# Kernel tuning notes

Measured on AMD Instinct MI355X. Metric: run time of the kernel, lower is better.

Reference implementation:

```python
import jax, jax.numpy as jnp
import numpy as np

EPS = 1e-5

def setup_inputs() -> dict:
    key = jax.random.key(0)
    ks = jax.random.split(key, 5)
    B, C_clip, Hc, Wc = 8, 768, 24, 24
    C_rs, Hr, Wr = 256, 64, 64
    clip_feat = jax.random.normal(ks[0], (B, C_clip, Hc, Wc), dtype=jnp.float32)
    rs_feat = jax.random.normal(ks[1], (B, C_rs, Hr, Wr), dtype=jnp.float32)
    ln_gamma = jnp.ones((C_clip,), dtype=jnp.float32)
    ln_beta = jnp.zeros((C_clip,), dtype=jnp.float32)
    W = jax.random.normal(ks[2], (C_rs, C_clip), dtype=jnp.float32) * (1.0 / np.sqrt(C_clip))
    b = jax.random.normal(ks[3], (C_rs,), dtype=jnp.float32) * 0.01
    alpha = jnp.array([0.5], dtype=jnp.float32)
    return {"clip_feat": clip_feat, "rs_feat": rs_feat, "ln_gamma": ln_gamma,
            "ln_beta": ln_beta, "W": W, "b": b, "alpha": alpha}

def reference(clip_feat, rs_feat, ln_gamma, ln_beta, W, b, alpha):
    B, C_clip, Hc, Wc = clip_feat.shape
    _, C_rs, Hr, Wr = rs_feat.shape
    # tokens: [B, N_clip, C_clip]
    clip_flat = clip_feat.reshape(B, C_clip, Hc * Wc).transpose(0, 2, 1)
    mu = jnp.mean(clip_flat, axis=-1, keepdims=True)
    var = jnp.var(clip_flat, axis=-1, keepdims=True)
    clip_norm = (clip_flat - mu) * jax.lax.rsqrt(var + EPS) * ln_gamma + ln_beta
    # projection to rs_dim: [B, N_clip, C_rs]
    clip_proj = jnp.einsum('bnc,dc->bnd', clip_norm, W) + b
    # rs tokens: [B, N_rs, C_rs]
    rs_flat = rs_feat.reshape(B, C_rs, Hr * Wr).transpose(0, 2, 1)
    # attn_map: [B, N_clip, N_rs], softmax over N_clip (axis=1)
    attn = jnp.einsum('bnd,bmd->bnm', clip_proj, rs_flat)
    attn = jax.nn.softmax(attn, axis=1)
    # attended: [B, N_rs, C_rs]
    attended = jnp.einsum('bnm,bnd->bmd', attn, clip_proj)
    attended = attended.transpose(0, 2, 1).reshape(B, C_rs, Hr, Wr)
    return rs_feat + alpha * attended
```

## Files before the change

### kernel.cpp

```cpp
#include <hip/hip_runtime.h>
#include <hip/hip_bf16.h>

#define EPSF 1e-5f
#define SM_OFF 60.0f

typedef short short8 __attribute__((ext_vector_type(8)));
typedef float f32x4 __attribute__((ext_vector_type(4)));

__device__ __forceinline__ short f2bf(float x) {
    __hip_bfloat16 h = __float2bfloat16(x);
    return reinterpret_cast<short&>(h);
}
__device__ __forceinline__ float bf2f(short s) {
    __hip_bfloat16 h = reinterpret_cast<__hip_bfloat16&>(s);
    return __bfloat162float(h);
}
__device__ __forceinline__ unsigned int pk2(float lo, float hi) {
    return (unsigned int)(unsigned short)f2bf(lo)
         | ((unsigned int)(unsigned short)f2bf(hi) << 16);
}
__device__ __forceinline__ void gload_lds16(const short* g, short* lds) {
    __builtin_amdgcn_global_load_lds(
        (const __attribute__((address_space(1))) unsigned int*)g,
        (__attribute__((address_space(3))) unsigned int*)lds,
        16, 0, 0);
}

__global__ __launch_bounds__(256) void w_pack_kernel(
    const float* __restrict__ W,
    short* __restrict__ Wp_hi,
    short* __restrict__ Wp_lo)
{
    int t = blockIdx.x * 256 + threadIdx.x;
    int l15 = t & 15;
    int g   = (t >> 4) & 3;
    int kt  = (t >> 6) % 24;
    int nt  = t / 1536;
    const float* src = W + (size_t)(16 * nt + l15) * 768 + 32 * kt + 8 * g;
    short8 h8, l8;
    #pragma unroll
    for (int j = 0; j < 8; ++j) {
        float w = src[j];
        short h = f2bf(w);
        h8[j] = h;
        l8[j] = f2bf(w - bf2f(h));
    }
    *reinterpret_cast<short8*>(Wp_hi + (size_t)t * 8) = h8;
    *reinterpret_cast<short8*>(Wp_lo + (size_t)t * 8) = l8;
}

__global__ __launch_bounds__(512) void ln_proj_kernel(
    const float* __restrict__ clip,
    const float* __restrict__ gamma,
    const float* __restrict__ beta,
    const short* __restrict__ Wp_hi,
    const short* __restrict__ Wp_lo,
    const float* __restrict__ bias,
    short* __restrict__ proj,
    short* __restrict__ projT)
{
    __shared__ short xh[16][776];
    __shared__ short xl[16][776];
    __shared__ float redA[8][16];
    __shared__ float redB[8][16];
    __shared__ float muS[16], rsS[16];

    const int tid = threadIdx.x;
    const int bb = blockIdx.x >> 1;
    const int dh = blockIdx.x & 1;
    const int b  = bb / 36;
    const int n0 = (bb % 36) * 16;
    const int nl = tid & 15;
    const int cg = tid >> 4;
    const int w  = tid >> 6;
    const int l  = tid & 63;
    const int l15 = l & 15;
    const int g  = l >> 4;

    const float* base = clip + (size_t)b * 768 * 576 + n0 + nl;

    float x[24];
    float s1 = 0.f, s2 = 0.f;
    #pragma unroll
    for (int i = 0; i < 24; ++i) {
        x[i] = base[(size_t)(cg + 32 * i) * 576];
        s1 += x[i]; s2 += x[i] * x[i];
    }
    s1 += __shfl_xor(s1, 16); s2 += __shfl_xor(s2, 16);
    s1 += __shfl_xor(s1, 32); s2 += __shfl_xor(s2, 32);
    if (g == 0) { redA[w][l15] = s1; redB[w][l15] = s2; }
    __syncthreads();
    if (tid < 16) {
        float a = 0.f, q = 0.f;
        #pragma unroll
        for (int k = 0; k < 8; ++k) { a += redA[k][tid]; q += redB[k][tid]; }
        float mu = a * (1.f / 768.f);
        float var = q * (1.f / 768.f) - mu * mu;
        muS[tid] = mu; rsS[tid] = rsqrtf(var + EPSF);
    }
    __syncthreads();
    {
        float mu = muS[nl], rsg = rsS[nl];
        #pragma unroll
        for (int i = 0; i < 24; ++i) {
            int c = cg + 32 * i;
            float y = (x[i] - mu) * rsg * gamma[c] + beta[c];
            short hh = f2bf(y);
            xh[nl][c] = hh;
            xl[nl][c] = f2bf(y - bf2f(hh));
        }
    }
    __syncthreads();

    const int nt = 8 * dh + w;
    f32x4 acc = f32x4{0.f, 0.f, 0.f, 0.f};
    for (int kt = 0; kt < 24; ++kt) {
        short8 ah = *reinterpret_cast<const short8*>(&xh[l15][32 * kt + 8 * g]);
        short8 al = *reinterpret_cast<const short8*>(&xl[l15][32 * kt + 8 * g]);
        size_t off = ((size_t)((nt * 24 + kt) * 64 + l)) * 8;
        short8 bh = *reinterpret_cast<const short8*>(Wp_hi + off);
        short8 bl = *reinterpret_cast<const short8*>(Wp_lo + off);
        acc = __builtin_amdgcn_mfma_f32_16x16x32_bf16(ah, bh, acc, 0, 0, 0);
        acc = __builtin_amdgcn_mfma_f32_16x16x32_bf16(al, bh, acc, 0, 0, 0);
        acc = __builtin_amdgcn_mfma_f32_16x16x32_bf16(ah, bl, acc, 0, 0, 0);
    }

    {
        int d = 16 * nt + l15;
        float bb2 = bias[d];
        #pragma unroll
        for (int r = 0; r < 4; ++r) {
            int tok = n0 + 4 * g + r;
            short v = f2bf(acc[r] + bb2);
            proj[((size_t)b * 576 + tok) * 256 + d] = v;
            projT[((size_t)b * 256 + d) * 576 + tok] = v;
        }
    }
}

__global__ __launch_bounds__(256, 4) void attn_kernel(
    const short* __restrict__ proj,
    const short* __restrict__ projT,
    const float* __restrict__ rs,
    const float* __restrict__ alpha_p,
    float* __restrict__ out)
{
    __shared__ short Ks[32][256];
    __shared__ short VT[128][32];
    __shared__ unsigned int Ps[4][16][20];

    const int tid = threadIdx.x;
    const int dh = blockIdx.x & 1;
    const int qt = (blockIdx.x >> 1) & 63;
    const int b  = blockIdx.x >> 7;
    const int q0 = qt << 6;
    const int w   = tid >> 6;
    const int l   = tid & 63;
    const int l15 = l & 15;
    const int g   = l >> 4;
    const int qg  = q0 + 16 * w + l15;

    const short* kbase  = proj  + (size_t)b * 576 * 256;
    const short* ktbase = projT + (size_t)b * 256 * 576;
    const float* rbase  = rs + (size_t)b * 256 * 4096;
    float* obase = out + (size_t)b * 256 * 4096;

    auto STAGE = [&](int c) {
        #pragma unroll
        for (int i = 0; i < 4; ++i) {
            int row0 = 8 * w + 2 * i;
            int rr = row0 + (l >> 5);
            const short* src = kbase + ((size_t)(32 * c + rr) << 8)
                             + ((((l & 31) ^ (rr & 7))) << 3);
            gload_lds16(src, &Ks[row0][0]);
        }
        #pragma unroll
        for (int i = 0; i < 2; ++i) {
            int d0 = 32 * w + 16 * i;
            int d = 128 * dh + d0 + (l >> 2);
            const short* src = ktbase + (size_t)d * 576 + 32 * c + 8 * (l & 3);
            gload_lds16(src, &VT[d0][0]);
        }
    };

    STAGE(0);
    short8 qf[8];
    #pragma unroll
    for (int dc = 0; dc < 8; ++dc) {
        short8 v;
        #pragma unroll
        for (int j = 0; j < 8; ++j)
            v[j] = f2bf(rbase[(size_t)(32 * dc + 8 * g + j) * 4096 + qg]);
        qf[dc] = v;
    }

    f32x4 acc[8];
    #pragma unroll
    for (int dt = 0; dt < 8; ++dt) acc[dt] = f32x4{0.f, 0.f, 0.f, 0.f};
    float rsum = 0.f;

    __syncthreads();

    for (int c = 0; c < 18; ++c) {
        f32x4 s0{0.f,0.f,0.f,0.f}, s1{0.f,0.f,0.f,0.f};
        __builtin_amdgcn_s_setprio(1);
        #pragma unroll
        for (int dc = 0; dc < 8; ++dc) {
            int sw = (((4 * dc + g) ^ (l15 & 7))) * 8;
            short8 kf0 = *reinterpret_cast<const short8*>(&Ks[l15][sw]);
            short8 kf1 = *reinterpret_cast<const short8*>(&Ks[16 + l15][sw]);
            s0 = __builtin_amdgcn_mfma_f32_16x16x32_bf16(kf0, qf[dc], s0, 0, 0, 0);
            s1 = __builtin_amdgcn_mfma_f32_16x16x32_bf16(kf1, qf[dc], s1, 0, 0, 0);
        }
        __builtin_amdgcn_s_setprio(0);

        float p[8];
        #pragma unroll
        for (int r = 0; r < 4; ++r) {
            p[r]     = __expf(s0[r] - SM_OFF);
            p[4 + r] = __expf(s1[r] - SM_OFF);
        }
        #pragma unroll
        for (int r = 0; r < 8; ++r) rsum += p[r];

        unsigned int u0 = pk2(p[0], p[1]), u1 = pk2(p[2], p[3]);
        unsigned int u2 = pk2(p[4], p[5]), u3 = pk2(p[6], p[7]);
        *reinterpret_cast<uint2*>(&Ps[w][l15][2 * g])     = uint2{u0, u1};
        *reinterpret_cast<uint2*>(&Ps[w][l15][8 + 2 * g]) = uint2{u2, u3};

        short8 pf = *reinterpret_cast<const short8*>(&Ps[w][l15][4 * g]);
        __builtin_amdgcn_s_setprio(1);
        #pragma unroll
        for (int dt = 0; dt < 8; ++dt) {
            short8 vf = *reinterpret_cast<const short8*>(&VT[16 * dt + l15][8 * g]);
            acc[dt] = __builtin_amdgcn_mfma_f32_16x16x32_bf16(vf, pf, acc[dt], 0, 0, 0);
        }
        __builtin_amdgcn_s_setprio(0);

        __syncthreads();
        if (c < 17) {
            STAGE(c + 1);
            __syncthreads();
        }
    }

    rsum += __shfl_xor(rsum, 16);
    rsum += __shfl_xor(rsum, 32);
    float inv = alpha_p[0] / rsum;

    #pragma unroll
    for (int dt = 0; dt < 8; ++dt) {
        #pragma unroll
        for (int r = 0; r < 4; ++r) {
            int d = 128 * dh + 16 * dt + 4 * g + r;
            size_t idx = (size_t)d * 4096 + qg;
            obase[idx] = rbase[idx] + acc[dt][r] * inv;
        }
    }
}

extern "C" void kernel_launch(void* const* d_in, const int* in_sizes, int n_in,
                              void* d_out, int out_size, void* d_ws, size_t ws_size,
                              hipStream_t stream)
{
    const float* clip  = (const float*)d_in[0];
    const float* rsf   = (const float*)d_in[1];
    const float* gamma = (const float*)d_in[2];
    const float* beta  = (const float*)d_in[3];
    const float* W     = (const float*)d_in[4];
    const float* bias  = (const float*)d_in[5];
    const float* alpha = (const float*)d_in[6];
    float* out = (float*)d_out;

    char* ws = (char*)d_ws;
    short* Wp_hi = (short*)ws;
    short* Wp_lo = (short*)(ws + 393216);
    short* proj  = (short*)(ws + 786432);
    short* projT = (short*)(ws + 3145728);

    hipLaunchKernelGGL(w_pack_kernel, dim3(96), dim3(256), 0, stream, W, Wp_hi, Wp_lo);
    hipLaunchKernelGGL(ln_proj_kernel, dim3(576), dim3(512), 0, stream,
                       clip, gamma, beta, Wp_hi, Wp_lo, bias, proj, projT);
    hipLaunchKernelGGL(attn_kernel, dim3(1024), dim3(256), 0, stream,
                       proj, projT, rsf, alpha, out);
}
```

Before: 79.02 us.

## Repartition attention block to share score tiles across waves covering all output dims

Each block now handles 32 queries across all 256 output channels instead of 64 queries over half the channels. Waves are split by query half and key half: each computes one 16x16 score tile and shares the probabilities through LDS. Each wave then accumulates its own 128-channel slice, and row sums are combined across waves through shared memory. This removes the duplicated QK score computation and exp work between the two channel-half blocks. In exchange it adds an extra block barrier per chunk, doubles the V tile staged per block, and loads each 32-query rs block twice (once per query-half wave pair).

```diff
diff --git a/kernel.cpp b/kernel.cpp
--- a/kernel.cpp
+++ b/kernel.cpp
@@ -146,19 +146,20 @@
     float* __restrict__ out)
 {
     __shared__ short Ks[32][256];
-    __shared__ short VT[128][32];
-    __shared__ unsigned int Ps[4][16][20];
+    __shared__ short VT[256][32];
+    __shared__ unsigned int Pb[2][16][20];
+    __shared__ float Rb[2][2][16];
 
     const int tid = threadIdx.x;
-    const int dh = blockIdx.x & 1;
-    const int qt = (blockIdx.x >> 1) & 63;
     const int b  = blockIdx.x >> 7;
-    const int q0 = qt << 6;
+    const int q0 = (blockIdx.x & 127) << 5;
     const int w   = tid >> 6;
     const int l   = tid & 63;
     const int l15 = l & 15;
     const int g   = l >> 4;
-    const int qg  = q0 + 16 * w + l15;
+    const int qh  = w >> 1;
+    const int kh  = w & 1;
+    const int qg  = q0 + 16 * qh + l15;
 
     const short* kbase  = proj  + (size_t)b * 576 * 256;
     const short* ktbase = projT + (size_t)b * 256 * 576;
@@ -175,9 +176,9 @@
             gload_lds16(src, &Ks[row0][0]);
         }
         #pragma unroll
-        for (int i = 0; i < 2; ++i) {
-            int d0 = 32 * w + 16 * i;
-            int d = 128 * dh + d0 + (l >> 2);
+        for (int i = 0; i < 4; ++i) {
+            int d0 = 64 * w + 16 * i;
+            int d = d0 + (l >> 2);
             const short* src = ktbase + (size_t)d * 576 + 32 * c + 8 * (l & 3);
             gload_lds16(src, &VT[d0][0]);
         }
@@ -202,37 +203,33 @@
     __syncthreads();
 
     for (int c = 0; c < 18; ++c) {
-        f32x4 s0{0.f,0.f,0.f,0.f}, s1{0.f,0.f,0.f,0.f};
+        f32x4 s{0.f, 0.f, 0.f, 0.f};
         __builtin_amdgcn_s_setprio(1);
         #pragma unroll
         for (int dc = 0; dc < 8; ++dc) {
             int sw = (((4 * dc + g) ^ (l15 & 7))) * 8;
-            short8 kf0 = *reinterpret_cast<const short8*>(&Ks[l15][sw]);
-            short8 kf1 = *reinterpret_cast<const short8*>(&Ks[16 + l15][sw]);
-            s0 = __builtin_amdgcn_mfma_f32_16x16x32_bf16(kf0, qf[dc], s0, 0, 0, 0);
-            s1 = __builtin_amdgcn_mfma_f32_16x16x32_bf16(kf1, qf[dc], s1, 0, 0, 0);
+            short8 kf = *reinterpret_cast<const short8*>(&Ks[16 * kh + l15][sw]);
+            s = __builtin_amdgcn_mfma_f32_16x16x32_bf16(kf, qf[dc], s, 0, 0, 0);
         }
         __builtin_amdgcn_s_setprio(0);
 
-        float p[8];
+        float p[4];
         #pragma unroll
         for (int r = 0; r < 4; ++r) {
-            p[r]     = __expf(s0[r] - SM_OFF);
-            p[4 + r] = __expf(s1[r] - SM_OFF);
-        }
-        #pragma unroll
-        for (int r = 0; r < 8; ++r) rsum += p[r];
-
-        unsigned int u0 = pk2(p[0], p[1]), u1 = pk2(p[2], p[3]);
-        unsigned int u2 = pk2(p[4], p[5]), u3 = pk2(p[6], p[7]);
-        *reinterpret_cast<uint2*>(&Ps[w][l15][2 * g])     = uint2{u0, u1};
-        *reinterpret_cast<uint2*>(&Ps[w][l15][8 + 2 * g]) = uint2{u2, u3};
-
-        short8 pf = *reinterpret_cast<const short8*>(&Ps[w][l15][4 * g]);
+            p[r] = __expf(s[r] - SM_OFF);
+            rsum += p[r];
+        }
+        *reinterpret_cast<uint2*>(&Pb[qh][l15][8 * kh + 2 * g]) =
+            uint2{pk2(p[0], p[1]), pk2(p[2], p[3])};
+
+        __syncthreads();
+
+        short8 pf = *reinterpret_cast<const short8*>(&Pb[qh][l15][4 * g]);
         __builtin_amdgcn_s_setprio(1);
         #pragma unroll
         for (int dt = 0; dt < 8; ++dt) {
-            short8 vf = *reinterpret_cast<const short8*>(&VT[16 * dt + l15][8 * g]);
+            short8 vf = *reinterpret_cast<const short8*>(
+                &VT[128 * kh + 16 * dt + l15][8 * g]);
             acc[dt] = __builtin_amdgcn_mfma_f32_16x16x32_bf16(vf, pf, acc[dt], 0, 0, 0);
         }
         __builtin_amdgcn_s_setprio(0);
@@ -246,13 +243,15 @@
 
     rsum += __shfl_xor(rsum, 16);
     rsum += __shfl_xor(rsum, 32);
-    float inv = alpha_p[0] / rsum;
+    if (g == 0) Rb[qh][kh][l15] = rsum;
+    __syncthreads();
+    float inv = alpha_p[0] / (Rb[qh][0][l15] + Rb[qh][1][l15]);
 
     #pragma unroll
     for (int dt = 0; dt < 8; ++dt) {
         #pragma unroll
         for (int r = 0; r < 4; ++r) {
-            int d = 128 * dh + 16 * dt + 4 * g + r;
+            int d = 128 * kh + 16 * dt + 4 * g + r;
             size_t idx = (size_t)d * 4096 + qg;
             obase[idx] = rbase[idx] + acc[dt][r] * inv;
         }
```

Result: faster. 76.09 us (-3.7%).
